# Kernel optimization log

Measured on AMD Instinct MI355X. Metric: run time of the kernel, lower is better.

Reference implementation:

```python
import jax, jax.numpy as jnp
import numpy as np

NEG_SLOPE = 0.2  # PyG GATConv default leaky_relu slope


def _gat_layer(x, src, dst, W, a_src, a_dst, b, N, concat):
    # x: [N, F_in]; W: [F_in, H*C]; a_src/a_dst: [H, C]; b: [H*C] or [C]
    H, C = a_src.shape
    h = (x @ W).reshape(N, H, C)                      # [N, H, C]
    al_s = jnp.einsum('nhc,hc->nh', h, a_src)          # [N, H]
    al_d = jnp.einsum('nhc,hc->nh', h, a_dst)          # [N, H]
    e = jax.nn.leaky_relu(al_s[src] + al_d[dst], NEG_SLOPE)  # [E, H]
    # segment softmax over incoming edges of each dst node
    m = jax.ops.segment_max(e, dst, num_segments=N)    # [N, H]
    ex = jnp.exp(e - m[dst])                           # [E, H]
    denom = jax.ops.segment_sum(ex, dst, num_segments=N)
    attn = ex / denom[dst]                             # [E, H]
    msg = (h[src] * attn[:, :, None]).reshape(-1, H * C)  # [E, H*C]
    out = jax.ops.segment_sum(msg, dst, num_segments=N)   # [N, H*C]
    if concat:
        return out + b
    return out.reshape(N, H, C).mean(axis=1) + b


def setup_inputs() -> dict:
    key = jax.random.key(0)
    ks = jax.random.split(key, 20)
    N, E, D, C, H = 20000, 160000, 768, 128, 4
    HC = H * C  # 512
    def glorot(k, shape):
        fan = shape[0] + shape[-1]
        return jax.random.uniform(k, shape, jnp.float32, -1.0, 1.0) * np.sqrt(6.0 / fan)
    inp = {
        'x': jax.random.normal(ks[0], (N, D), jnp.float32),
        'edge_index': jax.random.randint(ks[1], (2, E), 0, N, jnp.int64),
        'W1': glorot(ks[2], (D, HC)),  'as1': glorot(ks[3], (H, C)), 'ad1': glorot(ks[4], (H, C)), 'b1': jnp.zeros((HC,), jnp.float32),
        'W2': glorot(ks[5], (HC, HC)), 'as2': glorot(ks[6], (H, C)), 'ad2': glorot(ks[7], (H, C)), 'b2': jnp.zeros((HC,), jnp.float32),
        'W3': glorot(ks[8], (HC, C)),  'as3': glorot(ks[9], (1, C)), 'ad3': glorot(ks[10], (1, C)), 'b3': jnp.zeros((C,), jnp.float32),
        'Ws1': glorot(ks[11], (C, C // 2)), 'bs1': jnp.zeros((C // 2,), jnp.float32),
        'Ws2': glorot(ks[12], (C // 2, 1)), 'bs2': jnp.zeros((1,), jnp.float32),
    }
    return inp


def reference(x, edge_index, W1, as1, ad1, b1, W2, as2, ad2, b2, W3, as3, ad3, b3, Ws1, bs1, Ws2, bs2):
    N = x.shape[0]
    loops = jnp.arange(N, dtype=edge_index.dtype)
    src = jnp.concatenate([edge_index[0], loops])  # add self-loops (PyG default)
    dst = jnp.concatenate([edge_index[1], loops])
    h = _gat_layer(x, src, dst, W1, as1, ad1, b1, N, concat=True)
    h = jax.nn.relu(h)  # dropout is identity in eval mode
    h = _gat_layer(h, src, dst, W2, as2, ad2, b2, N, concat=True)
    h = jax.nn.relu(h)
    h = _gat_layer(h, src, dst, W3, as3, ad3, b3, N, concat=False)
    # risk scoring head: Linear -> ReLU -> Linear -> Sigmoid
    s = jax.nn.relu(h @ Ws1 + bs1)
    return jax.nn.sigmoid(s @ Ws2 + bs2)  # [N, 1]
```

## Files before the change

### kernel.cpp

```cpp
#include <hip/hip_runtime.h>
#include <hip/hip_bf16.h>
#include <math.h>

#define NEG_SLOPE 0.2f

typedef __attribute__((ext_vector_type(8))) __bf16 bf16x8;
typedef __attribute__((ext_vector_type(4))) float f32x4;

__device__ inline float lrelu(float v) { return v > 0.f ? v : NEG_SLOPE * v; }

__device__ inline unsigned short f2bf(float f) {
    __hip_bfloat16 h = __float2bfloat16(f);
    return *reinterpret_cast<unsigned short*>(&h);
}
__device__ inline float bf_lo(unsigned u) { return __uint_as_float(u << 16); }
__device__ inline float bf_hi(unsigned u) { return __uint_as_float(u & 0xffff0000u); }

__device__ inline void transpose_one(const float* __restrict__ in,
                                     unsigned short* __restrict__ out,
                                     int K, int N, int idx) {
    if (idx >= K * N) return;
    int n = idx / K, k = idx % K;
    out[(size_t)n * K + k] = f2bf(in[(size_t)k * N + n]);
}

__global__ __launch_bounds__(256) void preproc_kernel(
    const float* __restrict__ x, unsigned short* __restrict__ xbf, int n4,
    const float* __restrict__ W1, unsigned short* __restrict__ W1t,
    const float* __restrict__ W2, unsigned short* __restrict__ W2t,
    const float* __restrict__ W3, unsigned short* __restrict__ W3t,
    const float* __restrict__ Ws1, unsigned short* __restrict__ Ws1t,
    const int* __restrict__ ei, int E, int N, int* __restrict__ deg,
    int c0, int c1, int c2, int c3, int c4,
    int D, int HC, int C) {
    int b = blockIdx.x;
    int t = threadIdx.x;
    if (b < c0) {
        int i = b * 256 + t;
        if (i < n4) {
            float4 v = reinterpret_cast<const float4*>(x)[i];
            ushort4 o;
            o.x = f2bf(v.x); o.y = f2bf(v.y); o.z = f2bf(v.z); o.w = f2bf(v.w);
            reinterpret_cast<ushort4*>(xbf)[i] = o;
        }
        return;
    }
    b -= c0;
    if (b < c1) { transpose_one(W1, W1t, D, HC, b * 256 + t); return; }
    b -= c1;
    if (b < c2) { transpose_one(W2, W2t, HC, HC, b * 256 + t); return; }
    b -= c2;
    if (b < c3) { transpose_one(W3, W3t, HC, C, b * 256 + t); return; }
    b -= c3;
    if (b < c4) { transpose_one(Ws1, Ws1t, 128, 64, b * 256 + t); return; }
    b -= c4;
    {
        int e = b * 256 + t;
        if (e < E + N) {
            int dst = (e < E) ? ei[E + e] : (e - E);
            atomicAdd(&deg[dst], 1);
        }
    }
}

__global__ void scan_kernel(const int* __restrict__ deg, int* __restrict__ off, int N) {
    __shared__ int sums[1024];
    int tid = threadIdx.x;
    int chunk = (N + 1023) / 1024;
    int start = tid * chunk;
    int end = start + chunk; if (end > N) end = N;
    int s = 0;
#pragma unroll 4
    for (int i = start; i < end && i < N; i++) s += deg[i];
    sums[tid] = s;
    __syncthreads();
    for (int d = 1; d < 1024; d <<= 1) {
        int v = 0;
        if (tid >= d) v = sums[tid - d];
        __syncthreads();
        if (tid >= d) sums[tid] += v;
        __syncthreads();
    }
    int prefix = (tid == 0) ? 0 : sums[tid - 1];
    int run = prefix;
#pragma unroll 4
    for (int i = start; i < end && i < N; i++) { off[i] = run; run += deg[i]; }
    if (tid == 1023) off[N] = sums[1023];
}

__global__ void scatter_kernel(const int* __restrict__ ei, int E, int N,
                               const int* __restrict__ off, int* __restrict__ cursor,
                               int* __restrict__ csr_src) {
    int e = blockIdx.x * blockDim.x + threadIdx.x;
    if (e >= E + N) return;
    int src, dst;
    if (e < E) { src = ei[e]; dst = ei[E + e]; }
    else       { src = dst = e - E; }
    int pos = off[dst] + atomicAdd(&cursor[dst], 1);
    csr_src[pos] = src;
}

template <int HEADS>
__global__ __launch_bounds__(256) void gemm_bf16_alpha(const unsigned short* __restrict__ A,
                                                       const unsigned short* __restrict__ Bt,
                                                       unsigned short* __restrict__ C,
                                                       int M, int N, int K, int rowTiles,
                                                       const float* __restrict__ a_src,
                                                       const float* __restrict__ a_dst,
                                                       float* __restrict__ alS,
                                                       float* __restrict__ alD) {
    __shared__ unsigned short Asl[64 * 64];
    __shared__ unsigned short Bsl[128 * 64];
    const int tid  = threadIdx.x;
    const int lane = tid & 63;
    const int wave = tid >> 6;

    int r, c;
    {
        int b = blockIdx.x;
        int colTiles = N >> 7;
        if (colTiles == 4) {
            int mainRows = rowTiles & ~7;
            int mainBlocks = mainRows * 4;
            if (b < mainBlocks) {
                int xcd = b & 7;
                c = (b >> 3) & 3;
                r = (b >> 5) * 8 + xcd;
            } else {
                int idx = b - mainBlocks;
                r = mainRows + (idx >> 2);
                c = idx & 3;
            }
        } else { r = b; c = 0; }
    }
    const int rowBase = r * 64;
    const int colBase = c * 128;
    const int wm = (wave & 1) * 32;
    const int wn = (wave >> 1) * 64;
    const int q   = lane >> 4;
    const int l16 = lane & 15;

    const int r0 = tid >> 3;
    const int cg = (tid & 7) ^ (r0 & 7);

    f32x4 acc[2][4] = {};

    for (int k0 = 0; k0 < K; k0 += 64) {
#pragma unroll
        for (int it = 0; it < 2; it++) {
            int s = it * 256 + tid;
            int rr = it * 32 + r0;
            int ga = rowBase + rr; if (ga >= M) ga = M - 1;
            const unsigned short* gpa = A + (size_t)ga * K + k0 + cg * 8;
            __builtin_amdgcn_global_load_lds(
                (const __attribute__((address_space(1))) void*)gpa,
                (__attribute__((address_space(3))) void*)&Asl[(size_t)s * 8],
                16, 0, 0);
        }
#pragma unroll
        for (int it = 0; it < 4; it++) {
            int s = it * 256 + tid;
            int rr = it * 32 + r0;
            const unsigned short* gpb = Bt + (size_t)(colBase + rr) * K + k0 + cg * 8;
            __builtin_amdgcn_global_load_lds(
                (const __attribute__((address_space(1))) void*)gpb,
                (__attribute__((address_space(3))) void*)&Bsl[(size_t)s * 8],
                16, 0, 0);
        }
        __syncthreads();

#pragma unroll
        for (int kh = 0; kh < 2; kh++) {
            bf16x8 af[2], bfv[4];
#pragma unroll
            for (int mi = 0; mi < 2; mi++) {
                int row = wm + mi * 16 + l16;
                int ch = (kh * 4 + q) ^ (row & 7);
                af[mi] = *reinterpret_cast<const bf16x8*>(&Asl[row * 64 + ch * 8]);
            }
#pragma unroll
            for (int ni = 0; ni < 4; ni++) {
                int row = wn + ni * 16 + l16;
                int ch = (kh * 4 + q) ^ (row & 7);
                bfv[ni] = *reinterpret_cast<const bf16x8*>(&Bsl[row * 64 + ch * 8]);
            }
#pragma unroll
            for (int mi = 0; mi < 2; mi++)
#pragma unroll
                for (int ni = 0; ni < 4; ni++)
                    acc[mi][ni] = __builtin_amdgcn_mfma_f32_16x16x32_bf16(af[mi], bfv[ni], acc[mi][ni], 0, 0, 0);
        }
        __syncthreads();
    }

    const int hIdx = colBase >> 7;
    const float* asl = a_src + hIdx * 128;
    const float* adl = a_dst + hIdx * 128;
    float acoef[4], dcoef[4];
#pragma unroll
    for (int ni = 0; ni < 4; ni++) {
        int cl = wn + ni * 16 + l16;
        acoef[ni] = asl[cl];
        dcoef[ni] = adl[cl];
    }

    float2* red = reinterpret_cast<float2*>(Asl);
    const int half = wn >> 6;

#pragma unroll
    for (int mi = 0; mi < 2; mi++) {
#pragma unroll
        for (int rr = 0; rr < 4; rr++) {
            int lrow = wm + mi * 16 + q * 4 + rr;
            int grow = rowBase + lrow;
            bool ok = grow < M;
            float vs = 0.f, vd = 0.f;
#pragma unroll
            for (int ni = 0; ni < 4; ni++) {
                float hv = acc[mi][ni][rr];
                vs += hv * acoef[ni];
                vd += hv * dcoef[ni];
                if (ok) {
                    int gcol = colBase + wn + ni * 16 + l16;
                    C[(size_t)grow * N + gcol] = f2bf(hv);
                }
            }
#pragma unroll
            for (int d = 1; d < 16; d <<= 1) {
                vs += __shfl_xor(vs, d);
                vd += __shfl_xor(vd, d);
            }
            if (l16 == 0) red[lrow * 2 + half] = make_float2(vs, vd);
        }
    }
    __syncthreads();
    if (tid < 64) {
        int grow = rowBase + tid;
        if (grow < M) {
            float2 a = red[tid * 2 + 0];
            float2 b = red[tid * 2 + 1];
            alS[(size_t)grow * HEADS + hIdx] = a.x + b.x;
            alD[(size_t)grow * HEADS + hIdx] = a.y + b.y;
        }
    }
}

template <int H, int C, int MODE>
__global__ __launch_bounds__(256) void gat_aggregate(const unsigned short* __restrict__ hb,
                                                     const float* __restrict__ alS,
                                                     const float* __restrict__ alD,
                                                     const int* __restrict__ off,
                                                     const int* __restrict__ csr_src,
                                                     const float* __restrict__ bias,
                                                     unsigned short* __restrict__ outbuf,
                                                     int N) {
    constexpr int HC = H * C;
    constexpr int PER = HC / 64;
    __shared__ int   sIdx[4][16];
    __shared__ float sW[4][64];

    int n = (blockIdx.x * blockDim.x + threadIdx.x) >> 6;
    int lane = threadIdx.x & 63;
    int wave = threadIdx.x >> 6;
    if (n >= N) return;
    int beg = off[n], end = off[n + 1];

    const int grp  = lane >> 4;
    const int slot = lane & 15;
    const int myh  = (H == 4) ? grp : 0;
    const float adh = alD[n * H + myh];
    const unsigned short* hbl = hb + (size_t)lane * PER;
    const float* sWrow = &sW[wave][grp * 16];

    float m = -1e30f, dn = 0.f;
    float acc0 = 0.f, acc1 = 0.f, acc2 = 0.f, acc3 = 0.f,
          acc4 = 0.f, acc5 = 0.f, acc6 = 0.f, acc7 = 0.f;

    for (int base = beg; base < end; base += 16) {
        int cnt = end - base; if (cnt > 16) cnt = 16;
        bool act = slot < cnt;
        int s_l = csr_src[act ? (base + slot) : base];
        float v = act ? lrelu(alS[s_l * H + myh] + adh) : -1e30f;

        float mc = v;
#pragma unroll
        for (int d = 1; d < 16; d <<= 1) mc = fmaxf(mc, __shfl_xor(mc, d));
        float pl = __expf(v - mc);
        float dc = pl;
#pragma unroll
        for (int d = 1; d < 16; d <<= 1) dc += __shfl_xor(dc, d);
        float nm = fmaxf(m, mc);
        float so = __expf(m - nm);
        float sc = __expf(mc - nm);
        dn = dn * so + dc * sc;
        m = nm;
        float wl = pl * sc;

        if (lane < 16) sIdx[wave][lane] = s_l;
        sW[wave][lane] = wl;

        acc0 *= so; acc1 *= so;
        if (PER == 8) {
            acc2 *= so; acc3 *= so; acc4 *= so; acc5 *= so;
            acc6 *= so; acc7 *= so;
        }

        int cntR = (cnt + 3) & ~3;

        if (PER == 8) {
            int4   sI = *reinterpret_cast<const int4*>(&sIdx[wave][0]);
            float4 wv = *reinterpret_cast<const float4*>(&sWrow[0]);
            uint4 gA0 = *reinterpret_cast<const uint4*>(hbl + (size_t)sI.x * HC);
            uint4 gA1 = *reinterpret_cast<const uint4*>(hbl + (size_t)sI.y * HC);
            uint4 gA2 = *reinterpret_cast<const uint4*>(hbl + (size_t)sI.z * HC);
            uint4 gA3 = *reinterpret_cast<const uint4*>(hbl + (size_t)sI.w * HC);
            for (int i = 0; i < cntR; i += 4) {
                int4 sI2 = {}; float4 wv2 = {};
                uint4 gB0 = {}, gB1 = {}, gB2 = {}, gB3 = {};
                if (i + 4 < cntR) {
                    sI2 = *reinterpret_cast<const int4*>(&sIdx[wave][i + 4]);
                    wv2 = *reinterpret_cast<const float4*>(&sWrow[i + 4]);
                    gB0 = *reinterpret_cast<const uint4*>(hbl + (size_t)sI2.x * HC);
                    gB1 = *reinterpret_cast<const uint4*>(hbl + (size_t)sI2.y * HC);
                    gB2 = *reinterpret_cast<const uint4*>(hbl + (size_t)sI2.z * HC);
                    gB3 = *reinterpret_cast<const uint4*>(hbl + (size_t)sI2.w * HC);
                }
#define CONSUME(G, W)                                                   \
                { uint4 rc = G; float w = W;                            \
                  acc0 += bf_lo(rc.x) * w; acc1 += bf_hi(rc.x) * w;     \
                  acc2 += bf_lo(rc.y) * w; acc3 += bf_hi(rc.y) * w;     \
                  acc4 += bf_lo(rc.z) * w; acc5 += bf_hi(rc.z) * w;     \
                  acc6 += bf_lo(rc.w) * w; acc7 += bf_hi(rc.w) * w; }
                CONSUME(gA0, wv.x); CONSUME(gA1, wv.y);
                CONSUME(gA2, wv.z); CONSUME(gA3, wv.w);
#undef CONSUME
                sI = sI2; wv = wv2;
                gA0 = gB0; gA1 = gB1; gA2 = gB2; gA3 = gB3;
            }
        } else {
            int4   sI = *reinterpret_cast<const int4*>(&sIdx[wave][0]);
            float4 wv = *reinterpret_cast<const float4*>(&sWrow[0]);
            unsigned gA0 = *reinterpret_cast<const unsigned*>(hbl + (size_t)sI.x * HC);
            unsigned gA1 = *reinterpret_cast<const unsigned*>(hbl + (size_t)sI.y * HC);
            unsigned gA2 = *reinterpret_cast<const unsigned*>(hbl + (size_t)sI.z * HC);
            unsigned gA3 = *reinterpret_cast<const unsigned*>(hbl + (size_t)sI.w * HC);
            for (int i = 0; i < cntR; i += 4) {
                int4 sI2 = {}; float4 wv2 = {};
                unsigned gB0 = 0, gB1 = 0, gB2 = 0, gB3 = 0;
                if (i + 4 < cntR) {
                    sI2 = *reinterpret_cast<const int4*>(&sIdx[wave][i + 4]);
                    wv2 = *reinterpret_cast<const float4*>(&sWrow[i + 4]);
                    gB0 = *reinterpret_cast<const unsigned*>(hbl + (size_t)sI2.x * HC);
                    gB1 = *reinterpret_cast<const unsigned*>(hbl + (size_t)sI2.y * HC);
                    gB2 = *reinterpret_cast<const unsigned*>(hbl + (size_t)sI2.z * HC);
                    gB3 = *reinterpret_cast<const unsigned*>(hbl + (size_t)sI2.w * HC);
                }
                acc0 += bf_lo(gA0) * wv.x; acc1 += bf_hi(gA0) * wv.x;
                acc0 += bf_lo(gA1) * wv.y; acc1 += bf_hi(gA1) * wv.y;
                acc0 += bf_lo(gA2) * wv.z; acc1 += bf_hi(gA2) * wv.z;
                acc0 += bf_lo(gA3) * wv.w; acc1 += bf_hi(gA3) * wv.w;
                sI = sI2; wv = wv2;
                gA0 = gB0; gA1 = gB1; gA2 = gB2; gA3 = gB3;
            }
        }
    }

    float invd = 1.f / dn;
    unsigned short* op = outbuf + (size_t)n * HC + lane * PER;
    const float* bp = bias + lane * PER;
    if (PER == 8) {
        float o0 = acc0 * invd + bp[0], o1 = acc1 * invd + bp[1];
        float o2 = acc2 * invd + bp[2], o3 = acc3 * invd + bp[3];
        float o4 = acc4 * invd + bp[4], o5 = acc5 * invd + bp[5];
        float o6 = acc6 * invd + bp[6], o7 = acc7 * invd + bp[7];
        if (MODE == 0) {
            o0 = fmaxf(o0, 0.f); o1 = fmaxf(o1, 0.f); o2 = fmaxf(o2, 0.f); o3 = fmaxf(o3, 0.f);
            o4 = fmaxf(o4, 0.f); o5 = fmaxf(o5, 0.f); o6 = fmaxf(o6, 0.f); o7 = fmaxf(o7, 0.f);
        }
        op[0] = f2bf(o0); op[1] = f2bf(o1); op[2] = f2bf(o2); op[3] = f2bf(o3);
        op[4] = f2bf(o4); op[5] = f2bf(o5); op[6] = f2bf(o6); op[7] = f2bf(o7);
    } else {
        float o0 = acc0 * invd + bp[0], o1 = acc1 * invd + bp[1];
        if (MODE == 0) { o0 = fmaxf(o0, 0.f); o1 = fmaxf(o1, 0.f); }
        op[0] = f2bf(o0); op[1] = f2bf(o1);
    }
}

__global__ __launch_bounds__(256) void head_mfma(const unsigned short* __restrict__ H3,
                                                 const unsigned short* __restrict__ W1t,
                                                 const float* __restrict__ bs1,
                                                 const float* __restrict__ Ws2,
                                                 const float* __restrict__ bs2,
                                                 float* __restrict__ out, int M) {
    __shared__ unsigned short Asl[128 * 128];
    __shared__ unsigned short Bsl[64 * 128];
    const int tid = threadIdx.x, lane = tid & 63, wave = tid >> 6;
    const int q = lane >> 4, l16 = lane & 15;
    const int rowBase = blockIdx.x * 128;
    const int r0 = tid >> 4;
    const int cg = (tid & 15) ^ (r0 & 7);

#pragma unroll
    for (int it = 0; it < 8; it++) {
        int s = it * 256 + tid;
        int r = it * 16 + r0;
        int ga = rowBase + r; if (ga >= M) ga = M - 1;
        const unsigned short* gp = H3 + (size_t)ga * 128 + cg * 8;
        __builtin_amdgcn_global_load_lds(
            (const __attribute__((address_space(1))) void*)gp,
            (__attribute__((address_space(3))) void*)&Asl[(size_t)s * 8], 16, 0, 0);
    }
#pragma unroll
    for (int it = 0; it < 4; it++) {
        int s = it * 256 + tid;
        int r = it * 16 + r0;
        const unsigned short* gp = W1t + (size_t)r * 128 + cg * 8;
        __builtin_amdgcn_global_load_lds(
            (const __attribute__((address_space(1))) void*)gp,
            (__attribute__((address_space(3))) void*)&Bsl[(size_t)s * 8], 16, 0, 0);
    }
    __syncthreads();

    const int wm = wave * 32;
    f32x4 acc[2][4] = {};
#pragma unroll
    for (int kh = 0; kh < 4; kh++) {
        bf16x8 af[2], bfv[4];
#pragma unroll
        for (int mi = 0; mi < 2; mi++) {
            int row = wm + mi * 16 + l16;
            int ch = (kh * 4 + q) ^ (row & 7);
            af[mi] = *reinterpret_cast<const bf16x8*>(&Asl[row * 128 + ch * 8]);
        }
#pragma unroll
        for (int ni = 0; ni < 4; ni++) {
            int row = ni * 16 + l16;
            int ch = (kh * 4 + q) ^ (row & 7);
            bfv[ni] = *reinterpret_cast<const bf16x8*>(&Bsl[row * 128 + ch * 8]);
        }
#pragma unroll
        for (int mi = 0; mi < 2; mi++)
#pragma unroll
            for (int ni = 0; ni < 4; ni++)
                acc[mi][ni] = __builtin_amdgcn_mfma_f32_16x16x32_bf16(af[mi], bfv[ni], acc[mi][ni], 0, 0, 0);
    }
    __syncthreads();

    float b1v[4], w2v[4];
#pragma unroll
    for (int ni = 0; ni < 4; ni++) {
        int cI = ni * 16 + l16;
        b1v[ni] = bs1[cI];
        w2v[ni] = Ws2[cI];
    }
    float* red = reinterpret_cast<float*>(Bsl);
#pragma unroll
    for (int mi = 0; mi < 2; mi++) {
#pragma unroll
        for (int r = 0; r < 4; r++) {
            int lrow = wm + mi * 16 + q * 4 + r;
            float p = 0.f;
#pragma unroll
            for (int ni = 0; ni < 4; ni++)
                p += fmaxf(acc[mi][ni][r] + b1v[ni], 0.f) * w2v[ni];
#pragma unroll
            for (int d = 1; d < 16; d <<= 1) p += __shfl_xor(p, d);
            if (l16 == 0) red[lrow] = p;
        }
    }
    __syncthreads();
    if (tid < 128) {
        int g = rowBase + tid;
        if (g < M) out[g] = 1.f / (1.f + __expf(-(red[tid] + bs2[0])));
    }
}

extern "C" void kernel_launch(void* const* d_in, const int* in_sizes, int n_in,
                              void* d_out, int out_size, void* d_ws, size_t ws_size,
                              hipStream_t stream) {
    const float* x   = (const float*)d_in[0];
    const int*   ei  = (const int*)d_in[1];
    const float* W1  = (const float*)d_in[2];
    const float* as1 = (const float*)d_in[3];
    const float* ad1 = (const float*)d_in[4];
    const float* b1  = (const float*)d_in[5];
    const float* W2  = (const float*)d_in[6];
    const float* as2 = (const float*)d_in[7];
    const float* ad2 = (const float*)d_in[8];
    const float* b2  = (const float*)d_in[9];
    const float* W3  = (const float*)d_in[10];
    const float* as3 = (const float*)d_in[11];
    const float* ad3 = (const float*)d_in[12];
    const float* b3  = (const float*)d_in[13];
    const float* Ws1 = (const float*)d_in[14];
    const float* bs1 = (const float*)d_in[15];
    const float* Ws2 = (const float*)d_in[16];
    const float* bs2 = (const float*)d_in[17];

    const int N = out_size;
    const int E = in_sizes[1] / 2;
    const int D = in_sizes[0] / N;
    const int HC = 512, H = 4, C = 128;
    const int Etot = E + N;

    char* p = (char*)d_ws;
    auto alloc = [&](size_t bytes) -> void* {
        void* q = (void*)p;
        p += (bytes + 255) & ~(size_t)255;
        return q;
    };
    char*  zbeg   = p;
    int*   deg    = (int*)alloc((size_t)N * 4);
    int*   cursor = (int*)alloc((size_t)N * 4);
    char*  zend   = p;
    float* alS1   = (float*)alloc((size_t)N * H * 4);
    float* alD1   = (float*)alloc((size_t)N * H * 4);
    float* alS2   = (float*)alloc((size_t)N * H * 4);
    float* alD2   = (float*)alloc((size_t)N * H * 4);
    float* alS3   = (float*)alloc((size_t)N * 4);
    float* alD3   = (float*)alloc((size_t)N * 4);
    int*   off    = (int*)alloc((size_t)(N + 1) * 4);
    int*   csr    = (int*)alloc((size_t)Etot * 4);
    unsigned short* hbuf = (unsigned short*)alloc((size_t)N * HC * 2);
    unsigned short* xbf  = (unsigned short*)alloc((size_t)N * D * 2);
    unsigned short* obf  = (unsigned short*)alloc((size_t)N * HC * 2);
    unsigned short* W1t  = (unsigned short*)alloc((size_t)D * HC * 2);
    unsigned short* W2t  = (unsigned short*)alloc((size_t)HC * HC * 2);
    unsigned short* W3t  = (unsigned short*)alloc((size_t)HC * C * 2);
    unsigned short* Ws1t = (unsigned short*)alloc((size_t)C * 64 * 2);

    hipMemsetAsync(zbeg, 0, (size_t)(zend - zbeg), stream);

    {
        int n4 = N * D / 4;
        int c0 = (n4 + 255) / 256;
        int c1 = (D * HC + 255) / 256;
        int c2 = (HC * HC + 255) / 256;
        int c3 = (HC * C + 255) / 256;
        int c4 = (128 * 64 + 255) / 256;
        int c5 = (Etot + 255) / 256;
        int total = c0 + c1 + c2 + c3 + c4 + c5;
        preproc_kernel<<<total, 256, 0, stream>>>(
            x, xbf, n4, W1, W1t, W2, W2t, W3, W3t, Ws1, Ws1t,
            ei, E, N, deg, c0, c1, c2, c3, c4, D, HC, C);
    }
    scan_kernel<<<1, 1024, 0, stream>>>(deg, off, N);
    scatter_kernel<<<(Etot + 255) / 256, 256, 0, stream>>>(ei, E, N, off, cursor, csr);

    int node_blocks = (N + 3) / 4;
    int rowTiles64 = (N + 63) / 64;
    int headTiles = (N + 127) / 128;

    gemm_bf16_alpha<4><<<rowTiles64 * 4, 256, 0, stream>>>(
        xbf, W1t, hbuf, N, HC, D, rowTiles64, as1, ad1, alS1, alD1);
    gat_aggregate<4, 128, 0><<<node_blocks, 256, 0, stream>>>(
        hbuf, alS1, alD1, off, csr, b1, obf, N);

    gemm_bf16_alpha<4><<<rowTiles64 * 4, 256, 0, stream>>>(
        obf, W2t, hbuf, N, HC, HC, rowTiles64, as2, ad2, alS2, alD2);
    gat_aggregate<4, 128, 0><<<node_blocks, 256, 0, stream>>>(
        hbuf, alS2, alD2, off, csr, b2, obf, N);

    gemm_bf16_alpha<1><<<rowTiles64, 256, 0, stream>>>(
        obf, W3t, hbuf, N, C, HC, rowTiles64, as3, ad3, alS3, alD3);
    gat_aggregate<1, 128, 2><<<node_blocks, 256, 0, stream>>>(
        hbuf, alS3, alD3, off, csr, b3, xbf, N);

    head_mfma<<<headTiles, 256, 0, stream>>>(xbf, Ws1t, bs1, Ws2, bs2, (float*)d_out, N);
}
```

Measured before the change: 301.0 us.

## Fold CSR scatter into first GEMM launch and unroll aggregation gather

Removes the separate scatter kernel and runs its work in extra leading blocks of the first GEMM launch, saving one launch and letting the scatter overlap with GEMM tiles. The aggregation inner loop over each 16-edge chunk is replaced by a fixed, unrolled three-buffer issue/consume schedule so more gather loads are in flight at once. This raises register pressure in the aggregate kernel and assumes a chunk holds at most 16 edges. The GEMM now carries extra parameters and a branch at block entry.

Result: slower. 308.5 us (+2.5%).

```diff
diff --git a/kernel.cpp b/kernel.cpp
--- a/kernel.cpp
+++ b/kernel.cpp
@@ -88,18 +88,6 @@
     if (tid == 1023) off[N] = sums[1023];
 }
 
-__global__ void scatter_kernel(const int* __restrict__ ei, int E, int N,
-                               const int* __restrict__ off, int* __restrict__ cursor,
-                               int* __restrict__ csr_src) {
-    int e = blockIdx.x * blockDim.x + threadIdx.x;
-    if (e >= E + N) return;
-    int src, dst;
-    if (e < E) { src = ei[e]; dst = ei[E + e]; }
-    else       { src = dst = e - E; }
-    int pos = off[dst] + atomicAdd(&cursor[dst], 1);
-    csr_src[pos] = src;
-}
-
 template <int HEADS>
 __global__ __launch_bounds__(256) void gemm_bf16_alpha(const unsigned short* __restrict__ A,
                                                        const unsigned short* __restrict__ Bt,
@@ -108,16 +96,34 @@
                                                        const float* __restrict__ a_src,
                                                        const float* __restrict__ a_dst,
                                                        float* __restrict__ alS,
-                                                       float* __restrict__ alD) {
+                                                       float* __restrict__ alD,
+                                                       int scatBlocks,
+                                                       const int* __restrict__ ei, int E,
+                                                       const int* __restrict__ off,
+                                                       int* __restrict__ cursor,
+                                                       int* __restrict__ csr_src) {
     __shared__ unsigned short Asl[64 * 64];
     __shared__ unsigned short Bsl[128 * 64];
     const int tid  = threadIdx.x;
+
+    if (blockIdx.x < scatBlocks) {
+        int e = blockIdx.x * 256 + tid;
+        if (e < E + M) {
+            int src, dst;
+            if (e < E) { src = ei[e]; dst = ei[E + e]; }
+            else       { src = dst = e - E; }
+            int pos = off[dst] + atomicAdd(&cursor[dst], 1);
+            csr_src[pos] = src;
+        }
+        return;
+    }
+
     const int lane = tid & 63;
     const int wave = tid >> 6;
 
     int r, c;
     {
-        int b = blockIdx.x;
+        int b = blockIdx.x - scatBlocks;
         int colTiles = N >> 7;
         if (colTiles == 4) {
             int mainRows = rowTiles & ~7;
@@ -308,60 +314,58 @@
         int cntR = (cnt + 3) & ~3;
 
         if (PER == 8) {
-            int4   sI = *reinterpret_cast<const int4*>(&sIdx[wave][0]);
-            float4 wv = *reinterpret_cast<const float4*>(&sWrow[0]);
-            uint4 gA0 = *reinterpret_cast<const uint4*>(hbl + (size_t)sI.x * HC);
-            uint4 gA1 = *reinterpret_cast<const uint4*>(hbl + (size_t)sI.y * HC);
-            uint4 gA2 = *reinterpret_cast<const uint4*>(hbl + (size_t)sI.z * HC);
-            uint4 gA3 = *reinterpret_cast<const uint4*>(hbl + (size_t)sI.w * HC);
-            for (int i = 0; i < cntR; i += 4) {
-                int4 sI2 = {}; float4 wv2 = {};
-                uint4 gB0 = {}, gB1 = {}, gB2 = {}, gB3 = {};
-                if (i + 4 < cntR) {
-                    sI2 = *reinterpret_cast<const int4*>(&sIdx[wave][i + 4]);
-                    wv2 = *reinterpret_cast<const float4*>(&sWrow[i + 4]);
-                    gB0 = *reinterpret_cast<const uint4*>(hbl + (size_t)sI2.x * HC);
-                    gB1 = *reinterpret_cast<const uint4*>(hbl + (size_t)sI2.y * HC);
-                    gB2 = *reinterpret_cast<const uint4*>(hbl + (size_t)sI2.z * HC);
-                    gB3 = *reinterpret_cast<const uint4*>(hbl + (size_t)sI2.w * HC);
-                }
-#define CONSUME(G, W)                                                   \
-                { uint4 rc = G; float w = W;                            \
-                  acc0 += bf_lo(rc.x) * w; acc1 += bf_hi(rc.x) * w;     \
-                  acc2 += bf_lo(rc.y) * w; acc3 += bf_hi(rc.y) * w;     \
-                  acc4 += bf_lo(rc.z) * w; acc5 += bf_hi(rc.z) * w;     \
-                  acc6 += bf_lo(rc.w) * w; acc7 += bf_hi(rc.w) * w; }
-                CONSUME(gA0, wv.x); CONSUME(gA1, wv.y);
-                CONSUME(gA2, wv.z); CONSUME(gA3, wv.w);
-#undef CONSUME
-                sI = sI2; wv = wv2;
-                gA0 = gB0; gA1 = gB1; gA2 = gB2; gA3 = gB3;
-            }
+            int4 sIa, sIb, sIc; float4 wva, wvb, wvc;
+            uint4 a0, a1, a2, a3, b0, b1, b2, b3, c0, c1, c2, c3;
+#define ISSUE8(SI, WV, B0, B1, B2, B3, G)                                        \
+            { SI = *reinterpret_cast<const int4*>(&sIdx[wave][(G) * 4]);         \
+              WV = *reinterpret_cast<const float4*>(&sWrow[(G) * 4]);            \
+              B0 = *reinterpret_cast<const uint4*>(hbl + (size_t)SI.x * HC);     \
+              B1 = *reinterpret_cast<const uint4*>(hbl + (size_t)SI.y * HC);     \
+              B2 = *reinterpret_cast<const uint4*>(hbl + (size_t)SI.z * HC);     \
+              B3 = *reinterpret_cast<const uint4*>(hbl + (size_t)SI.w * HC); }
+#define CONS1(B, W)                                                              \
+            { acc0 += bf_lo(B.x) * W; acc1 += bf_hi(B.x) * W;                    \
+              acc2 += bf_lo(B.y) * W; acc3 += bf_hi(B.y) * W;                    \
+              acc4 += bf_lo(B.z) * W; acc5 += bf_hi(B.z) * W;                    \
+              acc6 += bf_lo(B.w) * W; acc7 += bf_hi(B.w) * W; }
+#define CONS48(WV, B0, B1, B2, B3)                                               \
+            { CONS1(B0, WV.x) CONS1(B1, WV.y) CONS1(B2, WV.z) CONS1(B3, WV.w) }
+            ISSUE8(sIa, wva, a0, a1, a2, a3, 0);
+            if (cntR > 4)  ISSUE8(sIb, wvb, b0, b1, b2, b3, 1);
+            CONS48(wva, a0, a1, a2, a3);
+            if (cntR > 8)  ISSUE8(sIc, wvc, c0, c1, c2, c3, 2);
+            if (cntR > 4)  CONS48(wvb, b0, b1, b2, b3);
+            if (cntR > 12) ISSUE8(sIa, wva, a0, a1, a2, a3, 3);
+            if (cntR > 8)  CONS48(wvc, c0, c1, c2, c3);
+            if (cntR > 12) CONS48(wva, a0, a1, a2, a3);
+#undef ISSUE8
+#undef CONS1
+#undef CONS48
         } else {
-            int4   sI = *reinterpret_cast<const int4*>(&sIdx[wave][0]);
-            float4 wv = *reinterpret_cast<const float4*>(&sWrow[0]);
-            unsigned gA0 = *reinterpret_cast<const unsigned*>(hbl + (size_t)sI.x * HC);
-            unsigned gA1 = *reinterpret_cast<const unsigned*>(hbl + (size_t)sI.y * HC);
-            unsigned gA2 = *reinterpret_cast<const unsigned*>(hbl + (size_t)sI.z * HC);
-            unsigned gA3 = *reinterpret_cast<const unsigned*>(hbl + (size_t)sI.w * HC);
-            for (int i = 0; i < cntR; i += 4) {
-                int4 sI2 = {}; float4 wv2 = {};
-                unsigned gB0 = 0, gB1 = 0, gB2 = 0, gB3 = 0;
-                if (i + 4 < cntR) {
-                    sI2 = *reinterpret_cast<const int4*>(&sIdx[wave][i + 4]);
-                    wv2 = *reinterpret_cast<const float4*>(&sWrow[i + 4]);
-                    gB0 = *reinterpret_cast<const unsigned*>(hbl + (size_t)sI2.x * HC);
-                    gB1 = *reinterpret_cast<const unsigned*>(hbl + (size_t)sI2.y * HC);
-                    gB2 = *reinterpret_cast<const unsigned*>(hbl + (size_t)sI2.z * HC);
-                    gB3 = *reinterpret_cast<const unsigned*>(hbl + (size_t)sI2.w * HC);
-                }
-                acc0 += bf_lo(gA0) * wv.x; acc1 += bf_hi(gA0) * wv.x;
-                acc0 += bf_lo(gA1) * wv.y; acc1 += bf_hi(gA1) * wv.y;
-                acc0 += bf_lo(gA2) * wv.z; acc1 += bf_hi(gA2) * wv.z;
-                acc0 += bf_lo(gA3) * wv.w; acc1 += bf_hi(gA3) * wv.w;
-                sI = sI2; wv = wv2;
-                gA0 = gB0; gA1 = gB1; gA2 = gB2; gA3 = gB3;
-            }
+            int4 sIa, sIb, sIc; float4 wva, wvb, wvc;
+            unsigned a0, a1, a2, a3, b0, b1, b2, b3, c0, c1, c2, c3;
+#define ISSUE2(SI, WV, B0, B1, B2, B3, G)                                        \
+            { SI = *reinterpret_cast<const int4*>(&sIdx[wave][(G) * 4]);         \
+              WV = *reinterpret_cast<const float4*>(&sWrow[(G) * 4]);            \
+              B0 = *reinterpret_cast<const unsigned*>(hbl + (size_t)SI.x * HC);  \
+              B1 = *reinterpret_cast<const unsigned*>(hbl + (size_t)SI.y * HC);  \
+              B2 = *reinterpret_cast<const unsigned*>(hbl + (size_t)SI.z * HC);  \
+              B3 = *reinterpret_cast<const unsigned*>(hbl + (size_t)SI.w * HC); }
+#define CONS42(WV, B0, B1, B2, B3)                                               \
+            { acc0 += bf_lo(B0) * WV.x; acc1 += bf_hi(B0) * WV.x;                \
+              acc0 += bf_lo(B1) * WV.y; acc1 += bf_hi(B1) * WV.y;                \
+              acc0 += bf_lo(B2) * WV.z; acc1 += bf_hi(B2) * WV.z;                \
+              acc0 += bf_lo(B3) * WV.w; acc1 += bf_hi(B3) * WV.w; }
+            ISSUE2(sIa, wva, a0, a1, a2, a3, 0);
+            if (cntR > 4)  ISSUE2(sIb, wvb, b0, b1, b2, b3, 1);
+            CONS42(wva, a0, a1, a2, a3);
+            if (cntR > 8)  ISSUE2(sIc, wvc, c0, c1, c2, c3, 2);
+            if (cntR > 4)  CONS42(wvb, b0, b1, b2, b3);
+            if (cntR > 12) ISSUE2(sIa, wva, a0, a1, a2, a3, 3);
+            if (cntR > 8)  CONS42(wvc, c0, c1, c2, c3);
+            if (cntR > 12) CONS42(wva, a0, a1, a2, a3);
+#undef ISSUE2
+#undef CONS42
         }
     }
 
@@ -545,24 +549,27 @@
             ei, E, N, deg, c0, c1, c2, c3, c4, D, HC, C);
     }
     scan_kernel<<<1, 1024, 0, stream>>>(deg, off, N);
-    scatter_kernel<<<(Etot + 255) / 256, 256, 0, stream>>>(ei, E, N, off, cursor, csr);
 
     int node_blocks = (N + 3) / 4;
     int rowTiles64 = (N + 63) / 64;
     int headTiles = (N + 127) / 128;
-
-    gemm_bf16_alpha<4><<<rowTiles64 * 4, 256, 0, stream>>>(
-        xbf, W1t, hbuf, N, HC, D, rowTiles64, as1, ad1, alS1, alD1);
+    int scatBlocks = (Etot + 255) / 256;
+
+    gemm_bf16_alpha<4><<<scatBlocks + rowTiles64 * 4, 256, 0, stream>>>(
+        xbf, W1t, hbuf, N, HC, D, rowTiles64, as1, ad1, alS1, alD1,
+        scatBlocks, ei, E, off, cursor, csr);
     gat_aggregate<4, 128, 0><<<node_blocks, 256, 0, stream>>>(
         hbuf, alS1, alD1, off, csr, b1, obf, N);
 
     gemm_bf16_alpha<4><<<rowTiles64 * 4, 256, 0, stream>>>(
-        obf, W2t, hbuf, N, HC, HC, rowTiles64, as2, ad2, alS2, alD2);
+        obf, W2t, hbuf, N, HC, HC, rowTiles64, as2, ad2, alS2, alD2,
+        0, nullptr, 0, nullptr, nullptr, nullptr);
     gat_aggregate<4, 128, 0><<<node_blocks, 256, 0, stream>>>(
         hbuf, alS2, alD2, off, csr, b2, obf, N);
 
     gemm_bf16_alpha<1><<<rowTiles64, 256, 0, stream>>>(
-        obf, W3t, hbuf, N, C, HC, rowTiles64, as3, ad3, alS3, alD3);
+        obf, W3t, hbuf, N, C, HC, rowTiles64, as3, ad3, alS3, alD3,
+        0, nullptr, 0, nullptr, nullptr, nullptr);
     gat_aggregate<1, 128, 2><<<node_blocks, 256, 0, stream>>>(
         hbuf, alS3, alD3, off, csr, b3, xbf, N);
 
```
